# Optimization experiments

Measured on AMD Instinct MI355X. Metric: run time of the kernel, lower is better.

The kernel has to match this reference:

```python
import jax, jax.numpy as jnp
import numpy as np

D_MODEL = 1024
N_HEADS = 16
DEPTH = D_MODEL // N_HEADS
B, S = 2, 2048
EPS_LN = 1e-6
EPS_KL = 2e-8


def _dense(x, W, b):
    return x @ W + b


def _ln(x, g, b):
    mu = jnp.mean(x, axis=-1, keepdims=True)
    var = jnp.mean(jnp.square(x - mu), axis=-1, keepdims=True)
    return (x - mu) * jax.lax.rsqrt(var + EPS_LN) * g + b


def _split_heads(x):
    # (B,S,D_MODEL) -> (B,H,S,DEPTH)
    return x.reshape(B, S, N_HEADS, DEPTH).transpose(0, 2, 1, 3)


def setup_inputs() -> dict:
    key = jax.random.key(0)
    ks = jax.random.split(key, 12)
    sc = 1.0 / np.sqrt(D_MODEL)
    inp = {
        'q_in': jax.random.normal(ks[0], (B, S, D_MODEL), jnp.float32),
        'k_in': jax.random.normal(ks[1], (B, S, D_MODEL), jnp.float32),
        'Wq': jax.random.normal(ks[2], (D_MODEL, D_MODEL), jnp.float32) * sc,
        'bq': jnp.zeros((D_MODEL,), jnp.float32),
        'Wk': jax.random.normal(ks[3], (D_MODEL, D_MODEL), jnp.float32) * sc,
        'bk': jnp.zeros((D_MODEL,), jnp.float32),
        'Wv': jax.random.normal(ks[4], (D_MODEL, D_MODEL), jnp.float32) * sc,
        'bv': jnp.zeros((D_MODEL,), jnp.float32),
        'Wo': jax.random.normal(ks[5], (D_MODEL, D_MODEL), jnp.float32) * sc,
        'bo': jnp.zeros((D_MODEL,), jnp.float32),
        'g1': jnp.ones((D_MODEL,), jnp.float32), 'b1': jnp.zeros((D_MODEL,), jnp.float32),
        'g2': jnp.ones((D_MODEL,), jnp.float32), 'b2': jnp.zeros((D_MODEL,), jnp.float32),
        'g3': jnp.ones((D_MODEL,), jnp.float32), 'b3': jnp.zeros((D_MODEL,), jnp.float32),
    }
    return inp


def reference(q_in, k_in, Wq, bq, Wk, bk, Wv, bv, Wo, bo, g1, b1, g2, b2, g3, b3):
    # Faithful to source: Wq applied twice to q, Wk twice to k, v = Wv(Wk(k_in))
    q = _ln(_dense(_dense(q_in, Wq, bq), Wq, bq), g1, b1)
    k1 = _dense(k_in, Wk, bk)
    k = _ln(_dense(k1, Wk, bk), g2, b2)
    v = _ln(_dense(k1, Wv, bv), g3, b3)

    q = _split_heads(q)   # (B,H,S,DEPTH)
    k = _split_heads(k)
    v = _split_heads(v)

    # KL-divergence attention scores.
    q_prob = jax.nn.softmax(q, axis=-1)
    k_prob = jax.nn.softmax(k, axis=-1)
    # sum_d q_prob*(log q_prob - log(k_prob+eps))
    # = [sum_d q_prob*log q_prob] - q_prob @ log(k_prob+eps)^T  (no 5D tensor)
    ent = jnp.sum(q_prob * jnp.log(q_prob), axis=-1)                     # (B,H,Sq)
    cross = jnp.einsum('bhqd,bhkd->bhqk', q_prob, jnp.log(k_prob + EPS_KL))
    kl_scores = ent[..., None] - cross                                   # (B,H,Sq,Sk)
    logits = kl_scores / jnp.sqrt(jnp.float32(DEPTH))

    # Csch softmax: csch(x)/sum csch(x)
    csch = 1.0 / jnp.sinh(logits)
    attn = csch / jnp.sum(csch, axis=-1, keepdims=True)                  # (B,H,Sq,Sk)

    out = jnp.einsum('bhqk,bhkd->bhqd', attn, v)
    out = out.transpose(0, 2, 1, 3).reshape(B, S, D_MODEL)
    output = _dense(out, Wo, bo)
    return output, attn
```

## Files before the change

kernel.cpp:

```cpp
#include <hip/hip_runtime.h>
#include <cstddef>
#include <cstdint>

#define BS      2
#define SEQ     2048
#define DM      1024
#define NH      16
#define DEPTH   64
#define ROWS    (BS*SEQ)
#define BHS     (BS*NH*SEQ)

typedef unsigned short u16;
typedef __attribute__((ext_vector_type(8))) short short8v;
typedef __attribute__((ext_vector_type(4))) float f32x4;

#define SWZ(row, cb) ((((row) << 7)) | ((cb) ^ (((row) & 7) << 4)))

__device__ __forceinline__ u16 f2bf(float x) {
    unsigned u = __builtin_bit_cast(unsigned, x);
    unsigned r = u + 0x7FFFu + ((u >> 16) & 1u);
    return (u16)(r >> 16);
}
__device__ __forceinline__ float bf2f(u16 h) {
    unsigned u = ((unsigned)h) << 16;
    return __builtin_bit_cast(float, u);
}

__device__ __forceinline__ float fast_csch(float x) {
    float t    = __expf(x);
    float den  = fmaf(t, t, -1.0f);
    bool  sm   = fabsf(x) < 0.04f;
    float d    = sm ? x : den;
    float r    = __builtin_amdgcn_rcpf(d);
    float big  = 2.0f * t * r;
    float smal = fmaf(x, -(1.0f/6.0f), r);
    return sm ? smal : big;
}

__global__ __launch_bounds__(256) void wprep_kernel(
    const float* __restrict__ W0, const float* __restrict__ W1,
    const float* __restrict__ W2_, const float* __restrict__ W3,
    const float* __restrict__ bq,
    u16* __restrict__ H0, u16* __restrict__ L0, u16* __restrict__ H1, u16* __restrict__ L1,
    u16* __restrict__ H2, u16* __restrict__ L2, u16* __restrict__ H3, u16* __restrict__ L3,
    u16* __restrict__ HN, u16* __restrict__ LN_, float* __restrict__ bq2)
{
    const int z = blockIdx.z;
    if (z == 4) {
        int bid = blockIdx.y * 32 + blockIdx.x;
        int i = bid * 256 + threadIdx.x;
        float4 v = ((const float4*)W0)[i];
        u16 h0 = f2bf(v.x), h1 = f2bf(v.y), h2 = f2bf(v.z), h3 = f2bf(v.w);
        u16 l0 = f2bf(v.x - bf2f(h0)), l1 = f2bf(v.y - bf2f(h1));
        u16 l2 = f2bf(v.z - bf2f(h2)), l3 = f2bf(v.w - bf2f(h3));
        uint2 hh, ll;
        hh.x = (unsigned)h0 | ((unsigned)h1 << 16); hh.y = (unsigned)h2 | ((unsigned)h3 << 16);
        ll.x = (unsigned)l0 | ((unsigned)l1 << 16); ll.y = (unsigned)l2 | ((unsigned)l3 << 16);
        ((uint2*)HN)[i] = hh;
        ((uint2*)LN_)[i] = ll;
        return;
    }
    if (z == 5) {
        if (blockIdx.y != 0 || blockIdx.x >= 16) return;
        __shared__ float part[4][64];
        const int t = threadIdx.x;
        const int nl = t & 63, kk = t >> 6;
        const int n = blockIdx.x * 64 + nl;
        float acc = 0.0f;
#pragma unroll 8
        for (int k = kk*256; k < kk*256 + 256; ++k)
            acc = fmaf(bq[k], W0[(size_t)k * DM + n], acc);
        part[kk][nl] = acc;
        __syncthreads();
        if (t < 64)
            bq2[blockIdx.x*64 + t] = part[0][t] + part[1][t] + part[2][t] + part[3][t]
                                   + bq[blockIdx.x*64 + t];
        return;
    }
    const float* W; u16* H; u16* L;
    switch (z) {
        case 0: W = W0; H = H0; L = L0; break;
        case 1: W = W1; H = H1; L = L1; break;
        case 2: W = W2_; H = H2; L = L2; break;
        default: W = W3; H = H3; L = L3; break;
    }
    __shared__ float tile[32][33];
    const int bn = blockIdx.x, bk = blockIdx.y;
    const int c = threadIdx.x & 31, r0 = threadIdx.x >> 5;
#pragma unroll
    for (int r = 0; r < 32; r += 8)
        tile[r0 + r][c] = W[(size_t)(bk*32 + r0 + r) * DM + bn*32 + c];
    __syncthreads();
#pragma unroll
    for (int r = 0; r < 32; r += 8) {
        float v = tile[c][r0 + r];
        u16 h = f2bf(v);
        size_t o = (size_t)(bn*32 + r0 + r) * DM + bk*32 + c;
        H[o] = h;
        L[o] = f2bf(v - bf2f(h));
    }
}

template<int OUT_MODE>
__global__ __launch_bounds__(256) void gemm_mfma(
    const u16* __restrict__ Ah, const u16* __restrict__ Al,
    const u16* __restrict__ Bh, const u16* __restrict__ Bl,
    const float* __restrict__ bias, float* __restrict__ C,
    u16* __restrict__ Ch, u16* __restrict__ Cl)
{
    constexpr int K = 1024, N = 1024;
    __shared__ u16 AsH[128*40], AsL[128*40], BsH[64*40], BsL[64*40];

    const int t = threadIdx.x;
    const int m0 = blockIdx.y * 128;
    const int n0 = blockIdx.x * 64;
    const int lane = t & 63, w = t >> 6;
    const int wr = w >> 1, wc = w & 1;
    const int lr = lane & 15, lk = lane >> 4;

    f32x4 acc[4][2];
#pragma unroll
    for (int i = 0; i < 4; ++i)
#pragma unroll
        for (int j = 0; j < 2; ++j) acc[i][j] = (f32x4){0.f,0.f,0.f,0.f};

    for (int k0 = 0; k0 < K; k0 += 32) {
        __syncthreads();
#pragma unroll
        for (int r = 0; r < 2; ++r) {
            int s = r*256 + t;
            int row = s >> 2, c = s & 3;
            size_t g = (size_t)(m0 + row) * K + k0 + c*8;
            *(short8v*)&AsH[row*40 + c*8] = *(const short8v*)&Ah[g];
            *(short8v*)&AsL[row*40 + c*8] = *(const short8v*)&Al[g];
        }
        {
            int row = t >> 2, c = t & 3;
            size_t g = (size_t)(n0 + row) * K + k0 + c*8;
            *(short8v*)&BsH[row*40 + c*8] = *(const short8v*)&Bh[g];
            *(short8v*)&BsL[row*40 + c*8] = *(const short8v*)&Bl[g];
        }
        __syncthreads();

        short8v ah[4], al[4], bh[2], bl[2];
#pragma unroll
        for (int i = 0; i < 4; ++i) {
            int off = (wr*64 + i*16 + lr)*40 + lk*8;
            ah[i] = *(const short8v*)&AsH[off];
            al[i] = *(const short8v*)&AsL[off];
        }
#pragma unroll
        for (int j = 0; j < 2; ++j) {
            int off = (wc*32 + j*16 + lr)*40 + lk*8;
            bh[j] = *(const short8v*)&BsH[off];
            bl[j] = *(const short8v*)&BsL[off];
        }
        __builtin_amdgcn_s_setprio(1);
#pragma unroll
        for (int i = 0; i < 4; ++i)
#pragma unroll
            for (int j = 0; j < 2; ++j) {
                acc[i][j] = __builtin_amdgcn_mfma_f32_16x16x32_bf16(ah[i], bh[j], acc[i][j], 0, 0, 0);
                acc[i][j] = __builtin_amdgcn_mfma_f32_16x16x32_bf16(ah[i], bl[j], acc[i][j], 0, 0, 0);
                acc[i][j] = __builtin_amdgcn_mfma_f32_16x16x32_bf16(al[i], bh[j], acc[i][j], 0, 0, 0);
            }
        __builtin_amdgcn_s_setprio(0);
    }

    float bj[2];
#pragma unroll
    for (int j = 0; j < 2; ++j) bj[j] = bias ? bias[n0 + wc*32 + j*16 + lr] : 0.0f;
#pragma unroll
    for (int i = 0; i < 4; ++i)
#pragma unroll
        for (int j = 0; j < 2; ++j) {
            int col = n0 + wc*32 + j*16 + lr;
#pragma unroll
            for (int r = 0; r < 4; ++r) {
                int row = m0 + wr*64 + i*16 + lk*4 + r;
                float v = acc[i][j][r] + bj[j];
                size_t o = (size_t)row * N + col;
                if constexpr (OUT_MODE == 0) {
                    C[o] = v;
                } else {
                    u16 h = f2bf(v);
                    Ch[o] = h;
                    Cl[o] = f2bf(v - bf2f(h));
                }
            }
        }
}

__global__ __launch_bounds__(256) void gemm_dual(
    const u16* __restrict__ Ah, const u16* __restrict__ Al,
    const u16* __restrict__ B0h, const u16* __restrict__ B0l,
    const u16* __restrict__ B1h, const u16* __restrict__ B1l,
    const float* __restrict__ bias0, const float* __restrict__ bias1,
    float* __restrict__ C0, float* __restrict__ C1)
{
    constexpr int K = 1024, N = 1024;
    __shared__ u16 AsH[128*40], AsL[128*40];
    __shared__ u16 B0H[64*40], B0L[64*40], B1H[64*40], B1L[64*40];

    const int t = threadIdx.x;
    const int m0 = blockIdx.y * 128;
    const int n0 = blockIdx.x * 64;
    const int lane = t & 63, w = t >> 6;
    const int wr = w >> 1, wc = w & 1;
    const int lr = lane & 15, lk = lane >> 4;

    f32x4 acc0[4][2], acc1[4][2];
#pragma unroll
    for (int i = 0; i < 4; ++i)
#pragma unroll
        for (int j = 0; j < 2; ++j) {
            acc0[i][j] = (f32x4){0.f,0.f,0.f,0.f};
            acc1[i][j] = (f32x4){0.f,0.f,0.f,0.f};
        }

    for (int k0 = 0; k0 < K; k0 += 32) {
        __syncthreads();
#pragma unroll
        for (int r = 0; r < 2; ++r) {
            int s = r*256 + t;
            int row = s >> 2, c = s & 3;
            size_t g = (size_t)(m0 + row) * K + k0 + c*8;
            *(short8v*)&AsH[row*40 + c*8] = *(const short8v*)&Ah[g];
            *(short8v*)&AsL[row*40 + c*8] = *(const short8v*)&Al[g];
        }
        {
            int row = t >> 2, c = t & 3;
            size_t g = (size_t)(n0 + row) * K + k0 + c*8;
            *(short8v*)&B0H[row*40 + c*8] = *(const short8v*)&B0h[g];
            *(short8v*)&B0L[row*40 + c*8] = *(const short8v*)&B0l[g];
            *(short8v*)&B1H[row*40 + c*8] = *(const short8v*)&B1h[g];
            *(short8v*)&B1L[row*40 + c*8] = *(const short8v*)&B1l[g];
        }
        __syncthreads();

        short8v ah[4], al[4];
#pragma unroll
        for (int i = 0; i < 4; ++i) {
            int off = (wr*64 + i*16 + lr)*40 + lk*8;
            ah[i] = *(const short8v*)&AsH[off];
            al[i] = *(const short8v*)&AsL[off];
        }
#pragma unroll
        for (int j = 0; j < 2; ++j) {
            int off = (wc*32 + j*16 + lr)*40 + lk*8;
            short8v b0h = *(const short8v*)&B0H[off];
            short8v b0l = *(const short8v*)&B0L[off];
            short8v b1h = *(const short8v*)&B1H[off];
            short8v b1l = *(const short8v*)&B1L[off];
            __builtin_amdgcn_s_setprio(1);
#pragma unroll
            for (int i = 0; i < 4; ++i) {
                acc0[i][j] = __builtin_amdgcn_mfma_f32_16x16x32_bf16(ah[i], b0h, acc0[i][j], 0, 0, 0);
                acc0[i][j] = __builtin_amdgcn_mfma_f32_16x16x32_bf16(ah[i], b0l, acc0[i][j], 0, 0, 0);
                acc0[i][j] = __builtin_amdgcn_mfma_f32_16x16x32_bf16(al[i], b0h, acc0[i][j], 0, 0, 0);
                acc1[i][j] = __builtin_amdgcn_mfma_f32_16x16x32_bf16(ah[i], b1h, acc1[i][j], 0, 0, 0);
                acc1[i][j] = __builtin_amdgcn_mfma_f32_16x16x32_bf16(ah[i], b1l, acc1[i][j], 0, 0, 0);
                acc1[i][j] = __builtin_amdgcn_mfma_f32_16x16x32_bf16(al[i], b1h, acc1[i][j], 0, 0, 0);
            }
            __builtin_amdgcn_s_setprio(0);
        }
    }

    float bj0[2], bj1[2];
#pragma unroll
    for (int j = 0; j < 2; ++j) {
        bj0[j] = bias0[n0 + wc*32 + j*16 + lr];
        bj1[j] = bias1[n0 + wc*32 + j*16 + lr];
    }
#pragma unroll
    for (int i = 0; i < 4; ++i)
#pragma unroll
        for (int j = 0; j < 2; ++j) {
            int col = n0 + wc*32 + j*16 + lr;
#pragma unroll
            for (int r = 0; r < 4; ++r) {
                int row = m0 + wr*64 + i*16 + lk*4 + r;
                size_t o = (size_t)row * N + col;
                C0[o] = acc0[i][j][r] + bj0[j];
                C1[o] = acc1[i][j][r] + bj1[j];
            }
        }
}

template<int OUT_MODE>
__global__ __launch_bounds__(256) void gemm_f32a(
    const float* __restrict__ A,
    const u16* __restrict__ Bh, const u16* __restrict__ Bl,
    const float* __restrict__ bias, float* __restrict__ C,
    u16* __restrict__ Ch, u16* __restrict__ Cl)
{
    constexpr int K = 1024, N = 1024;
    __shared__ u16 AsH[128*40], AsL[128*40], BsH[64*40], BsL[64*40];

    const int t = threadIdx.x;
    const int m0 = blockIdx.y * 128;
    const int n0 = blockIdx.x * 64;
    const int lane = t & 63, w = t >> 6;
    const int wr = w >> 1, wc = w & 1;
    const int lr = lane & 15, lk = lane >> 4;

    f32x4 acc[4][2];
#pragma unroll
    for (int i = 0; i < 4; ++i)
#pragma unroll
        for (int j = 0; j < 2; ++j) acc[i][j] = (f32x4){0.f,0.f,0.f,0.f};

    for (int k0 = 0; k0 < K; k0 += 32) {
        __syncthreads();
#pragma unroll
        for (int r = 0; r < 2; ++r) {
            int j = r*256 + t;
            int row = j >> 2, c8 = j & 3;
            const float* src = &A[(size_t)(m0 + row) * K + k0 + c8*8];
            float4 a = *(const float4*)src;
            float4 b = *(const float4*)(src + 4);
            float xs[8] = {a.x,a.y,a.z,a.w,b.x,b.y,b.z,b.w};
            short8v hv, lv;
#pragma unroll
            for (int jj = 0; jj < 8; ++jj) {
                u16 h = f2bf(xs[jj]);
                hv[jj] = (short)h;
                lv[jj] = (short)f2bf(xs[jj] - bf2f(h));
            }
            *(short8v*)&AsH[row*40 + c8*8] = hv;
            *(short8v*)&AsL[row*40 + c8*8] = lv;
        }
        {
            int row = t >> 2, c = t & 3;
            size_t g = (size_t)(n0 + row) * K + k0 + c*8;
            *(short8v*)&BsH[row*40 + c*8] = *(const short8v*)&Bh[g];
            *(short8v*)&BsL[row*40 + c*8] = *(const short8v*)&Bl[g];
        }
        __syncthreads();

        short8v ah[4], al[4], bh[2], bl[2];
#pragma unroll
        for (int i = 0; i < 4; ++i) {
            int off = (wr*64 + i*16 + lr)*40 + lk*8;
            ah[i] = *(const short8v*)&AsH[off];
            al[i] = *(const short8v*)&AsL[off];
        }
#pragma unroll
        for (int j = 0; j < 2; ++j) {
            int off = (wc*32 + j*16 + lr)*40 + lk*8;
            bh[j] = *(const short8v*)&BsH[off];
            bl[j] = *(const short8v*)&BsL[off];
        }
        __builtin_amdgcn_s_setprio(1);
#pragma unroll
        for (int i = 0; i < 4; ++i)
#pragma unroll
            for (int j = 0; j < 2; ++j) {
                acc[i][j] = __builtin_amdgcn_mfma_f32_16x16x32_bf16(ah[i], bh[j], acc[i][j], 0, 0, 0);
                acc[i][j] = __builtin_amdgcn_mfma_f32_16x16x32_bf16(ah[i], bl[j], acc[i][j], 0, 0, 0);
                acc[i][j] = __builtin_amdgcn_mfma_f32_16x16x32_bf16(al[i], bh[j], acc[i][j], 0, 0, 0);
            }
        __builtin_amdgcn_s_setprio(0);
    }

    float bj[2];
#pragma unroll
    for (int j = 0; j < 2; ++j) bj[j] = bias ? bias[n0 + wc*32 + j*16 + lr] : 0.0f;
#pragma unroll
    for (int i = 0; i < 4; ++i)
#pragma unroll
        for (int j = 0; j < 2; ++j) {
            int col = n0 + wc*32 + j*16 + lr;
#pragma unroll
            for (int r = 0; r < 4; ++r) {
                int row = m0 + wr*64 + i*16 + lk*4 + r;
                float v = acc[i][j][r] + bj[j];
                size_t o = (size_t)row * N + col;
                if constexpr (OUT_MODE == 0) {
                    C[o] = v;
                } else {
                    u16 h = f2bf(v);
                    Ch[o] = h;
                    Cl[o] = f2bf(v - bf2f(h));
                }
            }
        }
}

__global__ __launch_bounds__(256) void ln3_kernel(
    const float* __restrict__ X0, const float* __restrict__ X1,
    const float* __restrict__ X2,
    const float* __restrict__ G0, const float* __restrict__ B0,
    const float* __restrict__ G1, const float* __restrict__ B1,
    const float* __restrict__ G2, const float* __restrict__ B2,
    u16* __restrict__ QA, u16* __restrict__ QB,
    u16* __restrict__ KA, u16* __restrict__ KB,
    u16* __restrict__ VA, float* __restrict__ ENT)
{
    const int mode = blockIdx.y;
    const float* X; const float* G; const float* Bt;
    if (mode == 0)      { X = X0; G = G0; Bt = B0; }
    else if (mode == 1) { X = X1; G = G1; Bt = B1; }
    else                { X = X2; G = G2; Bt = B2; }

    const int row = blockIdx.x;
    const int tid = threadIdx.x;
    const float* x = X + (size_t)row * DM;
    float4 v = *(const float4*)&x[tid*4];

    float s  = v.x + v.y + v.z + v.w;
    float ss = v.x*v.x + v.y*v.y + v.z*v.z + v.w*v.w;
#pragma unroll
    for (int m = 1; m < 64; m <<= 1) { s += __shfl_xor(s, m); ss += __shfl_xor(ss, m); }
    __shared__ float redS[4], redQ[4];
    const int wave = tid >> 6, lane = tid & 63;
    if (lane == 0) { redS[wave] = s; redQ[wave] = ss; }
    __syncthreads();
    s  = redS[0] + redS[1] + redS[2] + redS[3];
    ss = redQ[0] + redQ[1] + redQ[2] + redQ[3];
    const float mu   = s * (1.0f / DM);
    const float var  = ss * (1.0f / DM) - mu * mu;
    const float rsig = rsqrtf(var + 1e-6f);

    float4 gv = *(const float4*)&G[tid*4];
    float4 bv = *(const float4*)&Bt[tid*4];
    float y0 = (v.x - mu) * rsig * gv.x + bv.x;
    float y1 = (v.y - mu) * rsig * gv.y + bv.y;
    float y2 = (v.z - mu) * rsig * gv.z + bv.z;
    float y3 = (v.w - mu) * rsig * gv.w + bv.w;

    const int b  = row >> 11;
    const int sl = row & (SEQ - 1);
    const int h  = tid >> 4;
    const size_t obase = (((size_t)(b*NH + h)) * SEQ + sl) * DEPTH + (tid & 15) * 4;

    if (mode == 2) {
        unsigned w0 = (unsigned)f2bf(y0) | ((unsigned)f2bf(y1) << 16);
        unsigned w1 = (unsigned)f2bf(y2) | ((unsigned)f2bf(y3) << 16);
        *(uint2*)&VA[obase] = make_uint2(w0, w1);
        return;
    }

    float mx = fmaxf(fmaxf(y0, y1), fmaxf(y2, y3));
#pragma unroll
    for (int m = 1; m < 16; m <<= 1) mx = fmaxf(mx, __shfl_xor(mx, m, 16));
    float e0 = expf(y0 - mx), e1 = expf(y1 - mx), e2 = expf(y2 - mx), e3 = expf(y3 - mx);
    float se = e0 + e1 + e2 + e3;
#pragma unroll
    for (int m = 1; m < 16; m <<= 1) se += __shfl_xor(se, m, 16);
    float inv = 1.0f / se;
    float p0 = e0*inv, p1 = e1*inv, p2 = e2*inv, p3 = e3*inv;
    float o0, o1, o2, o3;
    u16* OA; u16* OB;
    if (mode == 0) { o0 = p0; o1 = p1; o2 = p2; o3 = p3; OA = QA; OB = QB; }
    else {
        o0 = logf(p0 + 2e-8f); o1 = logf(p1 + 2e-8f);
        o2 = logf(p2 + 2e-8f); o3 = logf(p3 + 2e-8f);
        OA = KA; OB = KB;
    }
    u16 h0 = f2bf(o0), h1 = f2bf(o1), h2 = f2bf(o2), h3 = f2bf(o3);
    unsigned w0 = (unsigned)h0 | ((unsigned)h1 << 16);
    unsigned w1 = (unsigned)h2 | ((unsigned)h3 << 16);
    *(uint2*)&OA[obase] = make_uint2(w0, w1);
    u16 l0 = f2bf(o0 - bf2f(h0)), l1 = f2bf(o1 - bf2f(h1));
    u16 l2 = f2bf(o2 - bf2f(h2)), l3 = f2bf(o3 - bf2f(h3));
    w0 = (unsigned)l0 | ((unsigned)l1 << 16);
    w1 = (unsigned)l2 | ((unsigned)l3 << 16);
    *(uint2*)&OB[obase] = make_uint2(w0, w1);

    if (mode == 0) {
        float lse = logf(se);
        float el = p0*(y0-mx-lse) + p1*(y1-mx-lse) + p2*(y2-mx-lse) + p3*(y3-mx-lse);
#pragma unroll
        for (int m = 1; m < 16; m <<= 1) el += __shfl_xor(el, m, 16);
        if ((tid & 15) == 0) ENT[((size_t)(b*NH + h)) * SEQ + sl] = el;
    }
}

__global__ __launch_bounds__(256) void vtrans_kernel(
    const u16* __restrict__ Vb, u16* __restrict__ VT)
{
    __shared__ u16 T[256*72];
    const int bh = blockIdx.y;
    const int s0 = blockIdx.x * 256;
    const int t  = threadIdx.x;
#pragma unroll
    for (int i = 0; i < 8; ++i) {
        int c = i*256 + t;
        int s = c >> 3, d0 = (c & 7) * 8;
        *(short8v*)&T[s*72 + d0] =
            *(const short8v*)&Vb[((size_t)bh*SEQ + s0 + s)*DEPTH + d0];
    }
    __syncthreads();
#pragma unroll
    for (int i = 0; i < 8; ++i) {
        int c = i*256 + t;
        int d = c >> 5, sl0 = (c & 31) * 8;
        short8v v;
#pragma unroll
        for (int j = 0; j < 8; ++j) v[j] = (short)T[(sl0 + j)*72 + d];
        *(short8v*)&VT[((size_t)bh*DEPTH + d)*SEQ + s0 + sl0] = v;
    }
}

__global__ __launch_bounds__(256, 4) void attn7_kernel(
    const u16* __restrict__ QPh, const u16* __restrict__ QPl,
    const u16* __restrict__ LKh, const u16* __restrict__ LKl,
    const u16* __restrict__ VT, const float* __restrict__ ENT,
    float* __restrict__ ATTN, u16* __restrict__ OH, u16* __restrict__ OL)
{
    const int wg   = blockIdx.x;
    const int wgid = (wg & 7) * 128 + (wg >> 3);
    const int bh   = wgid >> 5;
    const int q0   = (wgid & 31) * 64;

    const int t  = threadIdx.x;
    const int l  = t & 63, w = t >> 6;
    const int lr = l & 15, lg = l >> 4;
    const size_t rbase = (size_t)bh * SEQ;

    __shared__ u16 KhS[64*64], KlS[64*64], VtS[64*64], PS[64*64];

    short8v qh[2], ql[2];
#pragma unroll
    for (int d = 0; d < 2; ++d) {
        size_t g = (rbase + q0 + w*16 + lr) * DEPTH + d*32 + lg*8;
        qh[d] = *(const short8v*)&QPh[g];
        ql[d] = *(const short8v*)&QPl[g];
    }
    float e8[4];
#pragma unroll
    for (int r = 0; r < 4; ++r)
        e8[r] = ENT[rbase + q0 + w*16 + lg*4 + r] * 0.125f;

    float rs[4] = {0.f, 0.f, 0.f, 0.f};
    for (int k0 = 0; k0 < SEQ; k0 += 64) {
        if (k0) __syncthreads();
#pragma unroll
        for (int r = 0; r < 2; ++r) {
            int s = r*256 + t; int kr = s >> 3, cb = (s & 7) * 16;
            size_t g = (rbase + k0 + kr) * DEPTH + (s & 7) * 8;
            *(short8v*)((char*)KhS + SWZ(kr, cb)) = *(const short8v*)&LKh[g];
            *(short8v*)((char*)KlS + SWZ(kr, cb)) = *(const short8v*)&LKl[g];
        }
        __syncthreads();

        f32x4 acc[4];
#pragma unroll
        for (int f = 0; f < 4; ++f) acc[f] = (f32x4){0.f,0.f,0.f,0.f};
        __builtin_amdgcn_s_setprio(1);
#pragma unroll
        for (int f = 0; f < 4; ++f)
#pragma unroll
            for (int d = 0; d < 2; ++d) {
                int off = SWZ(f*16 + lr, d*64 + lg*16);
                short8v kbh = *(const short8v*)((const char*)KhS + off);
                short8v kbl = *(const short8v*)((const char*)KlS + off);
                acc[f] = __builtin_amdgcn_mfma_f32_16x16x32_bf16(qh[d], kbh, acc[f], 0, 0, 0);
                acc[f] = __builtin_amdgcn_mfma_f32_16x16x32_bf16(qh[d], kbl, acc[f], 0, 0, 0);
                acc[f] = __builtin_amdgcn_mfma_f32_16x16x32_bf16(ql[d], kbh, acc[f], 0, 0, 0);
            }
        __builtin_amdgcn_s_setprio(0);
#pragma unroll
        for (int f = 0; f < 4; ++f)
#pragma unroll
            for (int r = 0; r < 4; ++r)
                rs[r] += fast_csch(fmaf(acc[f][r], -0.125f, e8[r]));
    }
#pragma unroll
    for (int m = 1; m < 16; m <<= 1)
#pragma unroll
        for (int r = 0; r < 4; ++r) rs[r] += __shfl_xor(rs[r], m, 16);
    float inv[4];
#pragma unroll
    for (int r = 0; r < 4; ++r) inv[r] = 1.0f / rs[r];

    f32x4 av[4];
#pragma unroll
    for (int nf = 0; nf < 4; ++nf) av[nf] = (f32x4){0.f,0.f,0.f,0.f};

    for (int k0 = 0; k0 < SEQ; k0 += 64) {
        __syncthreads();
#pragma unroll
        for (int r = 0; r < 2; ++r) {
            int s = r*256 + t; int kr = s >> 3, cb = (s & 7) * 16;
            size_t g = (rbase + k0 + kr) * DEPTH + (s & 7) * 8;
            *(short8v*)((char*)KhS + SWZ(kr, cb)) = *(const short8v*)&LKh[g];
            *(short8v*)((char*)KlS + SWZ(kr, cb)) = *(const short8v*)&LKl[g];
        }
#pragma unroll
        for (int r = 0; r < 2; ++r) {
            int s = r*256 + t; int dd = s >> 3, cb = (s & 7) * 16;
            *(short8v*)((char*)VtS + SWZ(dd, cb)) =
                *(const short8v*)&VT[((size_t)bh * DEPTH + dd) * SEQ + k0 + (s & 7) * 8];
        }
        __syncthreads();

        f32x4 acc[4];
#pragma unroll
        for (int f = 0; f < 4; ++f) acc[f] = (f32x4){0.f,0.f,0.f,0.f};
        __builtin_amdgcn_s_setprio(1);
#pragma unroll
        for (int f = 0; f < 4; ++f)
#pragma unroll
            for (int d = 0; d < 2; ++d) {
                int off = SWZ(f*16 + lr, d*64 + lg*16);
                short8v kbh = *(const short8v*)((const char*)KhS + off);
                short8v kbl = *(const short8v*)((const char*)KlS + off);
                acc[f] = __builtin_amdgcn_mfma_f32_16x16x32_bf16(qh[d], kbh, acc[f], 0, 0, 0);
                acc[f] = __builtin_amdgcn_mfma_f32_16x16x32_bf16(qh[d], kbl, acc[f], 0, 0, 0);
                acc[f] = __builtin_amdgcn_mfma_f32_16x16x32_bf16(ql[d], kbh, acc[f], 0, 0, 0);
            }
        __builtin_amdgcn_s_setprio(0);

#pragma unroll
        for (int f = 0; f < 4; ++f)
#pragma unroll
            for (int r = 0; r < 4; ++r) {
                float c = fast_csch(fmaf(acc[f][r], -0.125f, e8[r]));
                float a = c * inv[r];
                int q = w*16 + lg*4 + r;
                __builtin_nontemporal_store(a, &ATTN[(rbase + q0 + q) * SEQ + k0 + f*16 + lr]);
                *(u16*)((char*)PS + SWZ(q, (f*16 + lr)*2)) = f2bf(a);
            }

        short8v pa[2];
#pragma unroll
        for (int ks = 0; ks < 2; ++ks)
            pa[ks] = *(const short8v*)((const char*)PS + SWZ(w*16 + lr, ks*64 + lg*16));
        __builtin_amdgcn_s_setprio(1);
#pragma unroll
        for (int nf = 0; nf < 4; ++nf)
#pragma unroll
            for (int ks = 0; ks < 2; ++ks) {
                short8v vb = *(const short8v*)((const char*)VtS + SWZ(nf*16 + lr, ks*64 + lg*16));
                av[nf] = __builtin_amdgcn_mfma_f32_16x16x32_bf16(pa[ks], vb, av[nf], 0, 0, 0);
            }
        __builtin_amdgcn_s_setprio(0);
    }

    const int b = bh >> 4, h = bh & (NH - 1);
#pragma unroll
    for (int nf = 0; nf < 4; ++nf)
#pragma unroll
        for (int r = 0; r < 4; ++r) {
            int q = w*16 + lg*4 + r;
            int d = nf*16 + lr;
            size_t o = ((size_t)(b * SEQ + q0 + q)) * DM + h * DEPTH + d;
            float v = av[nf][r];
            u16 hh = f2bf(v);
            OH[o] = hh;
            OL[o] = f2bf(v - bf2f(hh));
        }
}

extern "C" void kernel_launch(void* const* d_in, const int* in_sizes, int n_in,
                              void* d_out, int out_size, void* d_ws, size_t ws_size,
                              hipStream_t stream)
{
    const float* q_in = (const float*)d_in[0];
    const float* k_in = (const float*)d_in[1];
    const float* Wq = (const float*)d_in[2];
    const float* bq = (const float*)d_in[3];
    const float* Wk = (const float*)d_in[4];
    const float* bk = (const float*)d_in[5];
    const float* Wv = (const float*)d_in[6];
    const float* bvp = (const float*)d_in[7];
    const float* Wo = (const float*)d_in[8];
    const float* bo = (const float*)d_in[9];
    const float* g1 = (const float*)d_in[10];
    const float* b1 = (const float*)d_in[11];
    const float* g2 = (const float*)d_in[12];
    const float* b2 = (const float*)d_in[13];
    const float* g3 = (const float*)d_in[14];
    const float* b3 = (const float*)d_in[15];

    float* out0 = (float*)d_out;
    float* attn = out0 + (size_t)ROWS * DM;

    char* base = (char*)d_ws;
    const size_t SLOT = (size_t)ROWS * DM * 4;
    const size_t HALF = (size_t)ROWS * DM;
    float* S0f = (float*)(base);
    float* S1f = (float*)(base + SLOT);
    float* S2f = (float*)(base + 2*SLOT);
    float* S3f = (float*)(base + 3*SLOT);
    u16* S0h = (u16*)S0f;
    u16* S3h = (u16*)S3f; u16* S3l = S3h + HALF;
    u16* QPh = (u16*)S3f; u16* QPl = QPh + HALF;
    u16* LKh = (u16*)S2f; u16* LKl = LKh + HALF;
    u16* Vb  = (u16*)S0f; u16* VTp = Vb + HALF;
    u16* OHp = (u16*)S1f; u16* OLp = OHp + HALF;
    u16* WqnH = S0h;
    u16* WqnL = S0h + (size_t)DM*DM;

    char* wbase = base + 4*SLOT;
    const size_t WSZ = (size_t)DM * DM * 2;
    u16* WqH = (u16*)(wbase);           u16* WqL = (u16*)(wbase + WSZ);
    u16* WkH = (u16*)(wbase + 2*WSZ);   u16* WkL = (u16*)(wbase + 3*WSZ);
    u16* WvH = (u16*)(wbase + 4*WSZ);   u16* WvL = (u16*)(wbase + 5*WSZ);
    u16* WoH = (u16*)(wbase + 6*WSZ);   u16* WoL = (u16*)(wbase + 7*WSZ);
    u16* W2H = (u16*)(wbase + 8*WSZ);   u16* W2L = (u16*)(wbase + 9*WSZ);
    float* ent = (float*)(wbase + 10*WSZ);
    float* bq2 = ent + BHS;

    const dim3 ggrid(DM/64, ROWS/128);
    const dim3 g2grid(DM/64, DM/128);

    wprep_kernel<<<dim3(32,32,6), 256, 0, stream>>>(
        Wq, Wk, Wv, Wo, bq,
        WqH, WqL, WkH, WkL, WvH, WvL, WoH, WoL, WqnH, WqnL, bq2);
    gemm_mfma<1><<<g2grid, 256, 0, stream>>>(WqH, WqL, WqnH, WqnL, nullptr,
                                             nullptr, W2H, W2L);

    gemm_f32a<0><<<ggrid, 256, 0, stream>>>(q_in, W2H, W2L, bq2, S2f, nullptr, nullptr);
    gemm_f32a<1><<<ggrid, 256, 0, stream>>>(k_in, WkH, WkL, bk, nullptr, S3h, S3l);
    gemm_dual<<<ggrid, 256, 0, stream>>>(S3h, S3l, WkH, WkL, WvH, WvL,
                                         bk, bvp, S0f, S1f);

    ln3_kernel<<<dim3(ROWS, 3), 256, 0, stream>>>(
        S2f, S0f, S1f, g1, b1, g2, b2, g3, b3,
        QPh, QPl, LKh, LKl, Vb, ent);
    vtrans_kernel<<<dim3(SEQ/256, BS*NH), 256, 0, stream>>>(Vb, VTp);

    attn7_kernel<<<dim3(SEQ/64 * BS*NH), 256, 0, stream>>>(
        QPh, QPl, LKh, LKl, VTp, ent, attn, OHp, OLp);

    gemm_mfma<0><<<ggrid, 256, 0, stream>>>(OHp, OLp, WoH, WoL, bo, out0, nullptr, nullptr);
}
```

Baseline: 500.2 us.

## Double attention query tile to 128 rows with 512-thread blocks sharing K/V tiles

Measured after the change: 530.5 us. +6.1%, slower.

```diff
diff --git a/kernel.cpp b/kernel.cpp
--- a/kernel.cpp
+++ b/kernel.cpp
@@ -503,23 +503,27 @@
     }
 }
 
-__global__ __launch_bounds__(256, 4) void attn7_kernel(
+__global__ __launch_bounds__(512, 4) void attn8_kernel(
     const u16* __restrict__ QPh, const u16* __restrict__ QPl,
     const u16* __restrict__ LKh, const u16* __restrict__ LKl,
     const u16* __restrict__ VT, const float* __restrict__ ENT,
     float* __restrict__ ATTN, u16* __restrict__ OH, u16* __restrict__ OL)
 {
     const int wg   = blockIdx.x;
-    const int wgid = (wg & 7) * 128 + (wg >> 3);
-    const int bh   = wgid >> 5;
-    const int q0   = (wgid & 31) * 64;
+    const int wgid = (wg & 7) * 64 + (wg >> 3);
+    const int bh   = wgid >> 4;
+    const int q0   = (wgid & 15) * 128;
 
     const int t  = threadIdx.x;
     const int l  = t & 63, w = t >> 6;
     const int lr = l & 15, lg = l >> 4;
     const size_t rbase = (size_t)bh * SEQ;
 
-    __shared__ u16 KhS[64*64], KlS[64*64], VtS[64*64], PS[64*64];
+    __shared__ u16 KhS[64*64], KlS[64*64], VtS[64*64];
+    __shared__ u16 PS[128*64];
+
+    const int kr = t >> 3, cc = t & 7;
+    const int wz = SWZ(kr, cc*16);
 
     short8v qh[2], ql[2];
 #pragma unroll
@@ -536,12 +540,10 @@
     float rs[4] = {0.f, 0.f, 0.f, 0.f};
     for (int k0 = 0; k0 < SEQ; k0 += 64) {
         if (k0) __syncthreads();
-#pragma unroll
-        for (int r = 0; r < 2; ++r) {
-            int s = r*256 + t; int kr = s >> 3, cb = (s & 7) * 16;
-            size_t g = (rbase + k0 + kr) * DEPTH + (s & 7) * 8;
-            *(short8v*)((char*)KhS + SWZ(kr, cb)) = *(const short8v*)&LKh[g];
-            *(short8v*)((char*)KlS + SWZ(kr, cb)) = *(const short8v*)&LKl[g];
+        {
+            size_t g = (rbase + k0 + kr) * DEPTH + cc*8;
+            *(short8v*)((char*)KhS + wz) = *(const short8v*)&LKh[g];
+            *(short8v*)((char*)KlS + wz) = *(const short8v*)&LKl[g];
         }
         __syncthreads();
 
@@ -581,18 +583,12 @@
 
     for (int k0 = 0; k0 < SEQ; k0 += 64) {
         __syncthreads();
-#pragma unroll
-        for (int r = 0; r < 2; ++r) {
-            int s = r*256 + t; int kr = s >> 3, cb = (s & 7) * 16;
-            size_t g = (rbase + k0 + kr) * DEPTH + (s & 7) * 8;
-            *(short8v*)((char*)KhS + SWZ(kr, cb)) = *(const short8v*)&LKh[g];
-            *(short8v*)((char*)KlS + SWZ(kr, cb)) = *(const short8v*)&LKl[g];
-        }
-#pragma unroll
-        for (int r = 0; r < 2; ++r) {
-            int s = r*256 + t; int dd = s >> 3, cb = (s & 7) * 16;
-            *(short8v*)((char*)VtS + SWZ(dd, cb)) =
-                *(const short8v*)&VT[((size_t)bh * DEPTH + dd) * SEQ + k0 + (s & 7) * 8];
+        {
+            size_t g = (rbase + k0 + kr) * DEPTH + cc*8;
+            *(short8v*)((char*)KhS + wz) = *(const short8v*)&LKh[g];
+            *(short8v*)((char*)KlS + wz) = *(const short8v*)&LKl[g];
+            *(short8v*)((char*)VtS + wz) =
+                *(const short8v*)&VT[((size_t)bh * DEPTH + kr) * SEQ + k0 + cc*8];
         }
         __syncthreads();
 
@@ -723,7 +719,7 @@
         QPh, QPl, LKh, LKl, Vb, ent);
     vtrans_kernel<<<dim3(SEQ/256, BS*NH), 256, 0, stream>>>(Vb, VTp);
 
-    attn7_kernel<<<dim3(SEQ/64 * BS*NH), 256, 0, stream>>>(
+    attn8_kernel<<<dim3(SEQ/128 * BS*NH), 512, 0, stream>>>(
         QPh, QPl, LKh, LKl, VTp, ent, attn, OHp, OLp);
 
     gemm_mfma<0><<<ggrid, 256, 0, stream>>>(OHp, OLp, WoH, WoL, bo, out0, nullptr, nullptr);
```
